# Performance work log

Hardware: AMD Instinct MI355X
Metric: run time of the kernel (lower is better)

Reference implementation:

```python
import jax, jax.numpy as jnp
import numpy as np

N_SEGMENTS = 16384

def setup_inputs() -> dict:
    key = jax.random.key(0)
    k1, k2, k3, k4 = jax.random.split(key, 4)
    N, D = 500000, 128
    x = jax.random.normal(k1, (N, D), dtype=jnp.float32)
    index = jnp.sort(jax.random.randint(k2, (N,), 0, N_SEGMENTS, dtype=jnp.int64))
    Wg = jax.random.normal(k3, (D, 1), dtype=jnp.float32) * 0.05
    bg = jnp.zeros((1,), dtype=jnp.float32)
    Wm = jax.random.normal(k4, (D, D), dtype=jnp.float32) * 0.05
    bm = jnp.zeros((D,), dtype=jnp.float32)
    return {"x": x, "index": index, "Wg": Wg, "bg": bg, "Wm": Wm, "bm": bm}

def reference(x, index, Wg, bg, Wm, bm):
    # gate_nn: Linear(d, 1)
    gate = x @ Wg + bg  # [N, 1]
    # segment softmax over nodes grouped by index (numerically stable)
    seg_max = jax.ops.segment_max(gate, index, num_segments=N_SEGMENTS)  # [S, 1]
    gate = jnp.exp(gate - seg_max[index])
    denom = jax.ops.segment_sum(gate, index, num_segments=N_SEGMENTS)[index] + 1e-10
    gate = gate / denom  # [N, 1]
    # message_nn: Linear(d, d)
    m = x @ Wm + bm  # [N, D]
    # weighted segment reduce
    out = jax.ops.segment_sum(gate * m, index, num_segments=N_SEGMENTS)  # [S, D]
    return out
```

## Files before the change

kernel.cpp:

```cpp
#include <hip/hip_runtime.h>

#define D 128

__device__ __forceinline__ int idx_at(const int* __restrict__ w, int n, bool is64) {
    return is64 ? w[2 * n] : w[n];
}

__global__ __launch_bounds__(256) void bounds_kernel(
    const int* __restrict__ w, int N, int S, int* __restrict__ segstart) {
    const int lane = threadIdx.x & 63;
    const int quarter = N >> 2;
    const int n0 = quarter + (int)(((long long)(quarter - 64) * lane) / 64);
    unsigned v = ((const unsigned*)w)[2 * n0 + 1];
#pragma unroll
    for (int m = 32; m; m >>= 1) v |= __shfl_xor(v, m, 64);
    const bool is64 = (v == 0u);
    const int s = blockIdx.x * blockDim.x + threadIdx.x;
    if (s > S) return;
    if (s == S) { segstart[S] = N; return; }
    int lo = 0, hi = N;
    while (lo < hi) {
        const int mid = (lo + hi) >> 1;
        if (idx_at(w, mid, is64) < s) lo = mid + 1; else hi = mid;
    }
    segstart[s] = lo;
}

__global__ __launch_bounds__(256) void seg_attn_kernel(
    const float* __restrict__ x, const int* __restrict__ segstart,
    const float* __restrict__ Wg, const float* __restrict__ bg,
    float* __restrict__ wx, float* __restrict__ segf, int S) {
    const int wid = threadIdx.x >> 6;
    const int lane = threadIdx.x & 63;
    const int s = blockIdx.x * 4 + wid;
    if (s >= S) return;
    const int start = segstart[s];
    const int end = segstart[s + 1];
    const int half = lane >> 5;
    const int c4 = (lane & 31) * 4;
    const float4 wg4 = *(const float4*)&Wg[c4];
    const float b0 = bg[0];
    float4 acc = {0.f, 0.f, 0.f, 0.f};
    float usum = 0.f;
    int r = start;
    for (; r + 8 <= end; r += 8) {
        const float4 a0 = *(const float4*)&x[(size_t)(r + 0 + half) * D + c4];
        const float4 a1 = *(const float4*)&x[(size_t)(r + 2 + half) * D + c4];
        const float4 a2 = *(const float4*)&x[(size_t)(r + 4 + half) * D + c4];
        const float4 a3 = *(const float4*)&x[(size_t)(r + 6 + half) * D + c4];
        float p0 = a0.x * wg4.x + a0.y * wg4.y + a0.z * wg4.z + a0.w * wg4.w;
        float p1 = a1.x * wg4.x + a1.y * wg4.y + a1.z * wg4.z + a1.w * wg4.w;
        float p2 = a2.x * wg4.x + a2.y * wg4.y + a2.z * wg4.z + a2.w * wg4.w;
        float p3 = a3.x * wg4.x + a3.y * wg4.y + a3.z * wg4.z + a3.w * wg4.w;
#pragma unroll
        for (int m = 1; m <= 16; m <<= 1) {
            p0 += __shfl_xor(p0, m, 64);
            p1 += __shfl_xor(p1, m, 64);
            p2 += __shfl_xor(p2, m, 64);
            p3 += __shfl_xor(p3, m, 64);
        }
        const float e0 = __expf(p0 + b0);
        const float e1 = __expf(p1 + b0);
        const float e2 = __expf(p2 + b0);
        const float e3 = __expf(p3 + b0);
        usum += (e0 + e1) + (e2 + e3);
        acc.x += e0 * a0.x + e1 * a1.x + e2 * a2.x + e3 * a3.x;
        acc.y += e0 * a0.y + e1 * a1.y + e2 * a2.y + e3 * a3.y;
        acc.z += e0 * a0.z + e1 * a1.z + e2 * a2.z + e3 * a3.z;
        acc.w += e0 * a0.w + e1 * a1.w + e2 * a2.w + e3 * a3.w;
    }
    for (; r < end; r += 2) {
        int row = r + half;
        if (row > end - 1) row = end - 1;
        const float4 a = *(const float4*)&x[(size_t)row * D + c4];
        float p = a.x * wg4.x + a.y * wg4.y + a.z * wg4.z + a.w * wg4.w;
#pragma unroll
        for (int m = 1; m <= 16; m <<= 1) p += __shfl_xor(p, m, 64);
        float e = __expf(p + b0);
        if (half && r + 1 >= end) e = 0.f;
        usum += e;
        acc.x += e * a.x;
        acc.y += e * a.y;
        acc.z += e * a.z;
        acc.w += e * a.w;
    }
    usum += __shfl_xor(usum, 32, 64);
    acc.x += __shfl_xor(acc.x, 32, 64);
    acc.y += __shfl_xor(acc.y, 32, 64);
    acc.z += __shfl_xor(acc.z, 32, 64);
    acc.w += __shfl_xor(acc.w, 32, 64);
    const float inv = 1.f / (usum + 1e-10f);
    if (half == 0) {
        float4 o;
        o.x = acc.x * inv;
        o.y = acc.y * inv;
        o.z = acc.z * inv;
        o.w = acc.w * inv;
        *(float4*)&wx[(size_t)s * D + c4] = o;
    }
    if (lane == 0) segf[s] = usum * inv;
}

__global__ __launch_bounds__(64) void gemm_kernel(
    float* __restrict__ out, const float* __restrict__ Wm,
    const float* __restrict__ bm, const float* __restrict__ segf) {
    __shared__ float tile[16 * 128];
    const int s0 = blockIdx.x * 16;
    const int tid = threadIdx.x;
    for (int t = tid; t < 16 * 128; t += 64) tile[t] = out[(size_t)s0 * 128 + t];
    __syncthreads();
    float2 acc[16];
#pragma unroll
    for (int r = 0; r < 16; ++r) { acc[r].x = 0.f; acc[r].y = 0.f; }
    for (int k = 0; k < 128; ++k) {
        const float2 wm = *(const float2*)&Wm[k * 128 + 2 * tid];
#pragma unroll
        for (int r = 0; r < 16; ++r) {
            const float wv = tile[r * 128 + k];
            acc[r].x += wv * wm.x;
            acc[r].y += wv * wm.y;
        }
    }
    const float2 bmv = *(const float2*)&bm[2 * tid];
#pragma unroll
    for (int r = 0; r < 16; ++r) {
        const int s = s0 + r;
        const float f = segf[s];
        float2 o;
        o.x = acc[r].x + f * bmv.x;
        o.y = acc[r].y + f * bmv.y;
        *(float2*)&out[(size_t)s * 128 + 2 * tid] = o;
    }
}

extern "C" void kernel_launch(void* const* d_in, const int* in_sizes, int n_in,
                              void* d_out, int out_size, void* d_ws, size_t ws_size,
                              hipStream_t stream) {
    const float* x  = (const float*)d_in[0];
    const int*   w  = (const int*)d_in[1];
    const float* Wg = (const float*)d_in[2];
    const float* bg = (const float*)d_in[3];
    const float* Wm = (const float*)d_in[4];
    const float* bm = (const float*)d_in[5];
    float* out = (float*)d_out;

    const int N = in_sizes[1];
    const int S = out_size / D;

    char* wsb = (char*)d_ws;
    int* segstart = (int*)wsb;
    float* segf = (float*)(segstart + S + 1);

    bounds_kernel<<<(S + 1 + 255) / 256, 256, 0, stream>>>(w, N, S, segstart);
    seg_attn_kernel<<<(S + 3) / 4, 256, 0, stream>>>(x, segstart, Wg, bg,
                                                     out, segf, S);
    gemm_kernel<<<S / 16, 64, 0, stream>>>(out, Wm, bm, segf);
}
```

Measured before the change: 399.0 us.

## Replace per-segment waves with balanced row-streaming and atomic segment flushes

Drops the binary-search bounds kernel and the one-wave-per-segment attention pass. A zero kernel now clears the output, then fixed row spans are streamed per wave with software prefetch of the next 8 rows, and partial sums are flushed with atomics whenever the segment id changes. Normalization by the exp-sum moves into the GEMM tile load. This balances load across waves regardless of segment size, at the cost of extra atomics, a per-row index read, and an extra zeroing pass. The max-shift stays absent, as before.

New measurement: 416.6 us. +4.4%, slower.

```diff
diff --git a/kernel.cpp b/kernel.cpp
--- a/kernel.cpp
+++ b/kernel.cpp
@@ -6,52 +6,60 @@
     return is64 ? w[2 * n] : w[n];
 }
 
-__global__ __launch_bounds__(256) void bounds_kernel(
-    const int* __restrict__ w, int N, int S, int* __restrict__ segstart) {
-    const int lane = threadIdx.x & 63;
+__global__ __launch_bounds__(256) void zero_kernel(float4* __restrict__ out4, int n4,
+                                                   float* __restrict__ usum, int S) {
+    const int i = blockIdx.x * blockDim.x + threadIdx.x;
+    const int stride = gridDim.x * blockDim.x;
+    for (int t = i; t < n4; t += stride) out4[t] = make_float4(0.f, 0.f, 0.f, 0.f);
+    for (int t = i; t < S; t += stride) usum[t] = 0.f;
+}
+
+__global__ __launch_bounds__(256) void stream_kernel(
+    const float* __restrict__ x, const int* __restrict__ w, int N, int span,
+    const float* __restrict__ Wg, const float* __restrict__ bg,
+    float* __restrict__ out, float* __restrict__ usum_g) {
+    const int tid = threadIdx.x;
+    const int wid = tid >> 6;
+    const int lane = tid & 63;
+    const int half = lane >> 5;
+    const int c4 = (lane & 31) * 4;
+
     const int quarter = N >> 2;
-    const int n0 = quarter + (int)(((long long)(quarter - 64) * lane) / 64);
-    unsigned v = ((const unsigned*)w)[2 * n0 + 1];
+    unsigned v = ((const unsigned*)w)[2 * (quarter + lane) + 1];
 #pragma unroll
     for (int m = 32; m; m >>= 1) v |= __shfl_xor(v, m, 64);
     const bool is64 = (v == 0u);
-    const int s = blockIdx.x * blockDim.x + threadIdx.x;
-    if (s > S) return;
-    if (s == S) { segstart[S] = N; return; }
-    int lo = 0, hi = N;
-    while (lo < hi) {
-        const int mid = (lo + hi) >> 1;
-        if (idx_at(w, mid, is64) < s) lo = mid + 1; else hi = mid;
-    }
-    segstart[s] = lo;
-}
 
-__global__ __launch_bounds__(256) void seg_attn_kernel(
-    const float* __restrict__ x, const int* __restrict__ segstart,
-    const float* __restrict__ Wg, const float* __restrict__ bg,
-    float* __restrict__ wx, float* __restrict__ segf, int S) {
-    const int wid = threadIdx.x >> 6;
-    const int lane = threadIdx.x & 63;
-    const int s = blockIdx.x * 4 + wid;
-    if (s >= S) return;
-    const int start = segstart[s];
-    const int end = segstart[s + 1];
-    const int half = lane >> 5;
-    const int c4 = (lane & 31) * 4;
+    const int wgid = blockIdx.x * 4 + wid;
+    const int r0 = wgid * span;
+    if (r0 >= N) return;
+    const int rend = min(r0 + span, N);
+
     const float4 wg4 = *(const float4*)&Wg[c4];
     const float b0 = bg[0];
+
     float4 acc = {0.f, 0.f, 0.f, 0.f};
-    float usum = 0.f;
-    int r = start;
-    for (; r + 8 <= end; r += 8) {
-        const float4 a0 = *(const float4*)&x[(size_t)(r + 0 + half) * D + c4];
-        const float4 a1 = *(const float4*)&x[(size_t)(r + 2 + half) * D + c4];
-        const float4 a2 = *(const float4*)&x[(size_t)(r + 4 + half) * D + c4];
-        const float4 a3 = *(const float4*)&x[(size_t)(r + 6 + half) * D + c4];
-        float p0 = a0.x * wg4.x + a0.y * wg4.y + a0.z * wg4.z + a0.w * wg4.w;
-        float p1 = a1.x * wg4.x + a1.y * wg4.y + a1.z * wg4.z + a1.w * wg4.w;
-        float p2 = a2.x * wg4.x + a2.y * wg4.y + a2.z * wg4.z + a2.w * wg4.w;
-        float p3 = a3.x * wg4.x + a3.y * wg4.y + a3.z * wg4.z + a3.w * wg4.w;
+    float us = 0.f;
+    int s_cur = -1;
+
+#define LDX(row) (*(const float4*)&x[(size_t)min((row), N - 1) * D + c4])
+
+    float4 c0 = LDX(r0 + 0 + half);
+    float4 c1 = LDX(r0 + 2 + half);
+    float4 c2 = LDX(r0 + 4 + half);
+    float4 c3 = LDX(r0 + 6 + half);
+
+    for (int r = r0; r < rend; r += 8) {
+        const int rn = (r + 8 < rend) ? (r + 8) : r;
+        float4 n0 = LDX(rn + 0 + half);
+        float4 n1 = LDX(rn + 2 + half);
+        float4 n2 = LDX(rn + 4 + half);
+        float4 n3 = LDX(rn + 6 + half);
+
+        float p0 = c0.x * wg4.x + c0.y * wg4.y + c0.z * wg4.z + c0.w * wg4.w;
+        float p1 = c1.x * wg4.x + c1.y * wg4.y + c1.z * wg4.z + c1.w * wg4.w;
+        float p2 = c2.x * wg4.x + c2.y * wg4.y + c2.z * wg4.z + c2.w * wg4.w;
+        float p3 = c3.x * wg4.x + c3.y * wg4.y + c3.z * wg4.z + c3.w * wg4.w;
 #pragma unroll
         for (int m = 1; m <= 16; m <<= 1) {
             p0 += __shfl_xor(p0, m, 64);
@@ -63,51 +71,65 @@
         const float e1 = __expf(p1 + b0);
         const float e2 = __expf(p2 + b0);
         const float e3 = __expf(p3 + b0);
-        usum += (e0 + e1) + (e2 + e3);
-        acc.x += e0 * a0.x + e1 * a1.x + e2 * a2.x + e3 * a3.x;
-        acc.y += e0 * a0.y + e1 * a1.y + e2 * a2.y + e3 * a3.y;
-        acc.z += e0 * a0.z + e1 * a1.z + e2 * a2.z + e3 * a3.z;
-        acc.w += e0 * a0.w + e1 * a1.w + e2 * a2.w + e3 * a3.w;
+
+#define PROC(i, ei, ci)                                                        \
+        {                                                                      \
+            const int row = r + 2 * (i) + half;                                \
+            if (row < rend) {                                                  \
+                const int si = idx_at(w, row, is64);                           \
+                if (si != s_cur) {                                             \
+                    if (s_cur >= 0) {                                          \
+                        float* o = &out[(size_t)s_cur * D + c4];               \
+                        atomicAdd(o + 0, acc.x);                               \
+                        atomicAdd(o + 1, acc.y);                               \
+                        atomicAdd(o + 2, acc.z);                               \
+                        atomicAdd(o + 3, acc.w);                               \
+                        if ((lane & 31) == 0) atomicAdd(&usum_g[s_cur], us);   \
+                    }                                                          \
+                    s_cur = si;                                                \
+                    acc.x = (ei) * (ci).x; acc.y = (ei) * (ci).y;              \
+                    acc.z = (ei) * (ci).z; acc.w = (ei) * (ci).w;              \
+                    us = (ei);                                                 \
+                } else {                                                       \
+                    acc.x += (ei) * (ci).x; acc.y += (ei) * (ci).y;            \
+                    acc.z += (ei) * (ci).z; acc.w += (ei) * (ci).w;            \
+                    us += (ei);                                                \
+                }                                                              \
+            }                                                                  \
+        }
+        PROC(0, e0, c0)
+        PROC(1, e1, c1)
+        PROC(2, e2, c2)
+        PROC(3, e3, c3)
+#undef PROC
+        c0 = n0; c1 = n1; c2 = n2; c3 = n3;
     }
-    for (; r < end; r += 2) {
-        int row = r + half;
-        if (row > end - 1) row = end - 1;
-        const float4 a = *(const float4*)&x[(size_t)row * D + c4];
-        float p = a.x * wg4.x + a.y * wg4.y + a.z * wg4.z + a.w * wg4.w;
-#pragma unroll
-        for (int m = 1; m <= 16; m <<= 1) p += __shfl_xor(p, m, 64);
-        float e = __expf(p + b0);
-        if (half && r + 1 >= end) e = 0.f;
-        usum += e;
-        acc.x += e * a.x;
-        acc.y += e * a.y;
-        acc.z += e * a.z;
-        acc.w += e * a.w;
+    if (s_cur >= 0) {
+        float* o = &out[(size_t)s_cur * D + c4];
+        atomicAdd(o + 0, acc.x);
+        atomicAdd(o + 1, acc.y);
+        atomicAdd(o + 2, acc.z);
+        atomicAdd(o + 3, acc.w);
+        if ((lane & 31) == 0) atomicAdd(&usum_g[s_cur], us);
     }
-    usum += __shfl_xor(usum, 32, 64);
-    acc.x += __shfl_xor(acc.x, 32, 64);
-    acc.y += __shfl_xor(acc.y, 32, 64);
-    acc.z += __shfl_xor(acc.z, 32, 64);
-    acc.w += __shfl_xor(acc.w, 32, 64);
-    const float inv = 1.f / (usum + 1e-10f);
-    if (half == 0) {
-        float4 o;
-        o.x = acc.x * inv;
-        o.y = acc.y * inv;
-        o.z = acc.z * inv;
-        o.w = acc.w * inv;
-        *(float4*)&wx[(size_t)s * D + c4] = o;
-    }
-    if (lane == 0) segf[s] = usum * inv;
+#undef LDX
 }
 
 __global__ __launch_bounds__(64) void gemm_kernel(
     float* __restrict__ out, const float* __restrict__ Wm,
-    const float* __restrict__ bm, const float* __restrict__ segf) {
+    const float* __restrict__ bm, const float* __restrict__ usum_g) {
     __shared__ float tile[16 * 128];
+    __shared__ float fseg[16];
     const int s0 = blockIdx.x * 16;
     const int tid = threadIdx.x;
-    for (int t = tid; t < 16 * 128; t += 64) tile[t] = out[(size_t)s0 * 128 + t];
+    for (int t = tid; t < 16 * 128; t += 64) {
+        const float u = usum_g[s0 + (t >> 7)];
+        tile[t] = out[(size_t)s0 * 128 + t] / (u + 1e-10f);
+    }
+    if (tid < 16) {
+        const float u = usum_g[s0 + tid];
+        fseg[tid] = u / (u + 1e-10f);
+    }
     __syncthreads();
     float2 acc[16];
 #pragma unroll
@@ -124,12 +146,11 @@
     const float2 bmv = *(const float2*)&bm[2 * tid];
 #pragma unroll
     for (int r = 0; r < 16; ++r) {
-        const int s = s0 + r;
-        const float f = segf[s];
+        const float f = fseg[r];
         float2 o;
         o.x = acc[r].x + f * bmv.x;
         o.y = acc[r].y + f * bmv.y;
-        *(float2*)&out[(size_t)s * 128 + 2 * tid] = o;
+        *(float2*)&out[(size_t)(s0 + r) * 128 + 2 * tid] = o;
     }
 }
 
@@ -147,12 +168,13 @@
     const int N = in_sizes[1];
     const int S = out_size / D;
 
-    char* wsb = (char*)d_ws;
-    int* segstart = (int*)wsb;
-    float* segf = (float*)(segstart + S + 1);
+    float* usum = (float*)d_ws;
 
-    bounds_kernel<<<(S + 1 + 255) / 256, 256, 0, stream>>>(w, N, S, segstart);
-    seg_attn_kernel<<<(S + 3) / 4, 256, 0, stream>>>(x, segstart, Wg, bg,
-                                                     out, segf, S);
-    gemm_kernel<<<S / 16, 64, 0, stream>>>(out, Wm, bm, segf);
+    const int nblocks = 1024;
+    const int waves = nblocks * 4;
+    const int span = (((N + waves - 1) / waves) + 1) & ~1;
+
+    zero_kernel<<<1024, 256, 0, stream>>>((float4*)out, out_size / 4, usum, S);
+    stream_kernel<<<nblocks, 256, 0, stream>>>(x, w, N, span, Wg, bg, out, usum);
+    gemm_kernel<<<S / 16, 64, 0, stream>>>(out, Wm, bm, usum);
 }
```

## Split gate computation into separate per-row kernel before segment accumulation

Applied to the files above, without the earlier changes.

Moves the gate dot product and exp out of the segment accumulation kernel into a new per-row kernel that writes exp(gate) to a workspace buffer. The accumulation kernel then reads precomputed gates instead of doing shuffle reductions. This removes the shuffle-reduction latency from the accumulation loop, but x (about 256 MB) is now read twice from memory. The gate kernel also uses one thread per row with strided, uncoalesced loads.

Result: slower. 436.2 us (+9.3%).

```diff
diff --git a/kernel.cpp b/kernel.cpp
--- a/kernel.cpp
+++ b/kernel.cpp
@@ -26,10 +26,39 @@
     segstart[s] = lo;
 }
 
-__global__ __launch_bounds__(256) void seg_attn_kernel(
-    const float* __restrict__ x, const int* __restrict__ segstart,
-    const float* __restrict__ Wg, const float* __restrict__ bg,
-    float* __restrict__ wx, float* __restrict__ segf, int S) {
+__global__ __launch_bounds__(256) void gate_kernel(
+    const float* __restrict__ x, const float* __restrict__ Wg,
+    const float* __restrict__ bg, float* __restrict__ g, int N) {
+    __shared__ float wg_s[D];
+    const int tid = threadIdx.x;
+    if (tid < D) wg_s[tid] = Wg[tid];
+    __syncthreads();
+    const int n = blockIdx.x * blockDim.x + tid;
+    if (n >= N) return;
+    const float4* __restrict__ xr = (const float4*)(x + (size_t)n * D);
+    const float4* __restrict__ wg4 = (const float4*)wg_s;
+    float4 acc0 = {0.f, 0.f, 0.f, 0.f};
+    float4 acc1 = {0.f, 0.f, 0.f, 0.f};
+#pragma unroll 4
+    for (int k = 0; k < 32; k += 2) {
+        const float4 a0 = xr[k];
+        const float4 a1 = xr[k + 1];
+        const float4 w0 = wg4[k];
+        const float4 w1 = wg4[k + 1];
+        acc0.x += a0.x * w0.x; acc0.y += a0.y * w0.y;
+        acc0.z += a0.z * w0.z; acc0.w += a0.w * w0.w;
+        acc1.x += a1.x * w1.x; acc1.y += a1.y * w1.y;
+        acc1.z += a1.z * w1.z; acc1.w += a1.w * w1.w;
+    }
+    const float dot = (acc0.x + acc0.y) + (acc0.z + acc0.w) +
+                      (acc1.x + acc1.y) + (acc1.z + acc1.w);
+    g[n] = __expf(dot + bg[0]);
+}
+
+__global__ __launch_bounds__(256) void accum_kernel(
+    const float* __restrict__ x, const float* __restrict__ g,
+    const int* __restrict__ segstart, float* __restrict__ wx,
+    float* __restrict__ segf, int S) {
     const int wid = threadIdx.x >> 6;
     const int lane = threadIdx.x & 63;
     const int s = blockIdx.x * 4 + wid;
@@ -38,32 +67,19 @@
     const int end = segstart[s + 1];
     const int half = lane >> 5;
     const int c4 = (lane & 31) * 4;
-    const float4 wg4 = *(const float4*)&Wg[c4];
-    const float b0 = bg[0];
     float4 acc = {0.f, 0.f, 0.f, 0.f};
-    float usum = 0.f;
+    float us = 0.f;
     int r = start;
     for (; r + 8 <= end; r += 8) {
         const float4 a0 = *(const float4*)&x[(size_t)(r + 0 + half) * D + c4];
         const float4 a1 = *(const float4*)&x[(size_t)(r + 2 + half) * D + c4];
         const float4 a2 = *(const float4*)&x[(size_t)(r + 4 + half) * D + c4];
         const float4 a3 = *(const float4*)&x[(size_t)(r + 6 + half) * D + c4];
-        float p0 = a0.x * wg4.x + a0.y * wg4.y + a0.z * wg4.z + a0.w * wg4.w;
-        float p1 = a1.x * wg4.x + a1.y * wg4.y + a1.z * wg4.z + a1.w * wg4.w;
-        float p2 = a2.x * wg4.x + a2.y * wg4.y + a2.z * wg4.z + a2.w * wg4.w;
-        float p3 = a3.x * wg4.x + a3.y * wg4.y + a3.z * wg4.z + a3.w * wg4.w;
-#pragma unroll
-        for (int m = 1; m <= 16; m <<= 1) {
-            p0 += __shfl_xor(p0, m, 64);
-            p1 += __shfl_xor(p1, m, 64);
-            p2 += __shfl_xor(p2, m, 64);
-            p3 += __shfl_xor(p3, m, 64);
-        }
-        const float e0 = __expf(p0 + b0);
-        const float e1 = __expf(p1 + b0);
-        const float e2 = __expf(p2 + b0);
-        const float e3 = __expf(p3 + b0);
-        usum += (e0 + e1) + (e2 + e3);
+        const float e0 = g[r + 0 + half];
+        const float e1 = g[r + 2 + half];
+        const float e2 = g[r + 4 + half];
+        const float e3 = g[r + 6 + half];
+        us += (e0 + e1) + (e2 + e3);
         acc.x += e0 * a0.x + e1 * a1.x + e2 * a2.x + e3 * a3.x;
         acc.y += e0 * a0.y + e1 * a1.y + e2 * a2.y + e3 * a3.y;
         acc.z += e0 * a0.z + e1 * a1.z + e2 * a2.z + e3 * a3.z;
@@ -73,23 +89,20 @@
         int row = r + half;
         if (row > end - 1) row = end - 1;
         const float4 a = *(const float4*)&x[(size_t)row * D + c4];
-        float p = a.x * wg4.x + a.y * wg4.y + a.z * wg4.z + a.w * wg4.w;
-#pragma unroll
-        for (int m = 1; m <= 16; m <<= 1) p += __shfl_xor(p, m, 64);
-        float e = __expf(p + b0);
+        float e = g[row];
         if (half && r + 1 >= end) e = 0.f;
-        usum += e;
+        us += e;
         acc.x += e * a.x;
         acc.y += e * a.y;
         acc.z += e * a.z;
         acc.w += e * a.w;
     }
-    usum += __shfl_xor(usum, 32, 64);
+    us += __shfl_xor(us, 32, 64);
     acc.x += __shfl_xor(acc.x, 32, 64);
     acc.y += __shfl_xor(acc.y, 32, 64);
     acc.z += __shfl_xor(acc.z, 32, 64);
     acc.w += __shfl_xor(acc.w, 32, 64);
-    const float inv = 1.f / (usum + 1e-10f);
+    const float inv = 1.f / (us + 1e-10f);
     if (half == 0) {
         float4 o;
         o.x = acc.x * inv;
@@ -98,7 +111,7 @@
         o.w = acc.w * inv;
         *(float4*)&wx[(size_t)s * D + c4] = o;
     }
-    if (lane == 0) segf[s] = usum * inv;
+    if (lane == 0) segf[s] = us * inv;
 }
 
 __global__ __launch_bounds__(64) void gemm_kernel(
@@ -150,9 +163,10 @@
     char* wsb = (char*)d_ws;
     int* segstart = (int*)wsb;
     float* segf = (float*)(segstart + S + 1);
+    float* g = (float*)(wsb + ((4 * (2 * S + 1) + 255) & ~255));
 
     bounds_kernel<<<(S + 1 + 255) / 256, 256, 0, stream>>>(w, N, S, segstart);
-    seg_attn_kernel<<<(S + 3) / 4, 256, 0, stream>>>(x, segstart, Wg, bg,
-                                                     out, segf, S);
+    gate_kernel<<<(N + 255) / 256, 256, 0, stream>>>(x, Wg, bg, g, N);
+    accum_kernel<<<(S + 3) / 4, 256, 0, stream>>>(x, g, segstart, out, segf, S);
     gemm_kernel<<<S / 16, 64, 0, stream>>>(out, Wm, bm, segf);
 }
```
